# Optimization experiments

Measured on AMD Instinct MI355X. Metric: run time of the kernel, lower is better.

Reference implementation:

```python
import jax, jax.numpy as jnp
import numpy as np

EMBED_DIM = 384
MAX_LEN = 5000
TIMESTEP = 10000.0


def _build_table():
    pos = np.arange(MAX_LEN, dtype=np.float32)[:, None]
    div = np.exp(np.arange(0, EMBED_DIM, 2, dtype=np.float32) * (-np.log(TIMESTEP) / EMBED_DIM))
    pe = np.zeros((MAX_LEN, EMBED_DIM), dtype=np.float32)
    pe[:, 0::2] = np.sin(pos * div)
    pe[:, 1::2] = np.cos(pos * div)
    return jnp.asarray(pe)


def setup_inputs() -> dict:
    key = jax.random.key(0)
    x = jax.random.randint(key, (32, 512), 0, 16, dtype=jnp.int32)  # per-token durations
    pos_enc = _build_table()  # (MAX_LEN, EMBED_DIM) learned-free sinusoidal table
    return {"x": x, "pos_enc": pos_enc}


def reference(x, pos_enc):
    # x: (B, N) int durations; output: (B, T, D), T = max row-total frames
    cs = jnp.cumsum(x, axis=1)                 # (B, N) cumulative frame counts
    total = cs[:, -1]                          # (B,) frames per row
    T = int(np.asarray(jnp.max(cs)))           # concrete max total frames (data-dep, eval eagerly)
    starts = cs - x                            # (B, N) start frame of each token
    t = jnp.arange(T, dtype=cs.dtype)          # (T,) frame indices
    # token owning each frame: first index with cs > t
    tok = jax.vmap(lambda c: jnp.searchsorted(c, t, side='right'))(cs)  # (B, T)
    tok = jnp.minimum(tok, x.shape[1] - 1)     # clamp for padded frames
    pos = t[None, :] - jnp.take_along_axis(starts, tok, axis=1)         # (B, T) within-token position
    valid = t[None, :] < total[:, None]        # (B, T)
    pos = jnp.where(valid, pos, 0)
    emb = pos_enc[pos]                         # (B, T, D) gather
    return emb * valid[..., None].astype(emb.dtype)
```

## Files before the change

### kernel.cpp

```cpp
#include <hip/hip_runtime.h>
#include <hip/hip_bf16.h>


#define B 32
#define L 512
#define D 384
#define D4 (D / 4)

__global__ __launch_bounds__(64) void pe_cumsum_kernel(
    const int* __restrict__ x, int* __restrict__ cs) {
  const int b = blockIdx.x;
  const int lane = threadIdx.x;
  const int base = b * L + lane * 8;

  const int4* xr = reinterpret_cast<const int4*>(x + base);
  int4 a = xr[0];
  int4 c = xr[1];
  int v[8] = {a.x, a.y, a.z, a.w, c.x, c.y, c.z, c.w};

  int pref[8];
  int s = 0;
#pragma unroll
  for (int k = 0; k < 8; ++k) { s += v[k]; pref[k] = s; }

  int acc = s;
#pragma unroll
  for (int off = 1; off < 64; off <<= 1) {
    int n = __shfl_up(acc, off);
    if (lane >= off) acc += n;
  }
  const int offset = acc - s;

  int4 o0 = make_int4(offset + pref[0], offset + pref[1],
                      offset + pref[2], offset + pref[3]);
  int4 o1 = make_int4(offset + pref[4], offset + pref[5],
                      offset + pref[6], offset + pref[7]);
  int4* cr = reinterpret_cast<int4*>(cs + base);
  cr[0] = o0;
  cr[1] = o1;
}

__global__ __launch_bounds__(256) void pe_searchsorted_kernel(
    const int* __restrict__ x, const int* __restrict__ cs,
    int* __restrict__ posidx, int T) {
  const int b = blockIdx.y;
  const int t = blockIdx.x * 256 + threadIdx.x;
  if (t >= T) return;

  const int* csr = cs + b * L;
  const int total = csr[L - 1];

  int out = -1;
  if (t < total) {
    int lo = 0, hi = L;
    while (lo < hi) {
      int mid = (lo + hi) >> 1;
      if (csr[mid] <= t) lo = mid + 1; else hi = mid;
    }
    int tok = lo < (L - 1) ? lo : (L - 1);
    out = t - (csr[tok] - x[b * L + tok]);
  }
  posidx[b * T + t] = out;
}

__global__ __launch_bounds__(256) void pe_gather_kernel(
    const float4* __restrict__ pe, const int* __restrict__ posidx,
    float4* __restrict__ out, int n4) {
  const int stride = gridDim.x * blockDim.x;
  for (int i = blockIdx.x * blockDim.x + threadIdx.x; i < n4; i += stride) {
    const int row = i / D4;
    const int col = i - row * D4;
    const int p = posidx[row];
    float4 v = make_float4(0.f, 0.f, 0.f, 0.f);
    if (p >= 0) v = pe[p * D4 + col];
    out[i] = v;
  }
}

extern "C" void kernel_launch(void* const* d_in, const int* in_sizes, int n_in,
                              void* d_out, int out_size, void* d_ws, size_t ws_size,
                              hipStream_t stream) {
  const int* x = (const int*)d_in[0];
  const float* pe = (const float*)d_in[1];
  float* out = (float*)d_out;

  const int T = out_size / (B * D);

  int* cs = (int*)d_ws;
  int* posidx = cs + B * L;

  pe_cumsum_kernel<<<B, 64, 0, stream>>>(x, cs);

  dim3 g2((T + 255) / 256, B);
  pe_searchsorted_kernel<<<g2, 256, 0, stream>>>(x, cs, posidx, T);

  const int n4 = out_size / 4;
  int blocks = (n4 + 255) / 256;
  if (blocks > 2048) blocks = 2048;
  pe_gather_kernel<<<blocks, 256, 0, stream>>>(
      (const float4*)pe, posidx, (float4*)out, n4);
}
```

Before: 200.9 us.

## Replace searchsorted+gather with per-token segment copy and tail zeroing

Instead of computing a per-frame token index by binary search and then gathering table rows, each (batch, token) block copies the first c rows of the positional table directly into that token's output segment. A separate kernel zeros the padded frames past each row's total. This removes the index buffer, the binary searches and the per-element index loads. It trades them for many small blocks with uneven work and unaligned segment starts.

```diff
diff --git a/kernel.cpp b/kernel.cpp
--- a/kernel.cpp
+++ b/kernel.cpp
@@ -40,40 +40,32 @@
   cr[1] = o1;
 }
 
-__global__ __launch_bounds__(256) void pe_searchsorted_kernel(
+__global__ __launch_bounds__(256) void pe_segcopy_kernel(
     const int* __restrict__ x, const int* __restrict__ cs,
-    int* __restrict__ posidx, int T) {
+    const float4* __restrict__ pe, float4* __restrict__ out, int T) {
+  const int j = blockIdx.x;
   const int b = blockIdx.y;
-  const int t = blockIdx.x * 256 + threadIdx.x;
-  if (t >= T) return;
+  const int c = x[b * L + j];
+  if (c == 0) return;
+  const int start = cs[b * L + j] - c;
 
-  const int* csr = cs + b * L;
-  const int total = csr[L - 1];
-
-  int out = -1;
-  if (t < total) {
-    int lo = 0, hi = L;
-    while (lo < hi) {
-      int mid = (lo + hi) >> 1;
-      if (csr[mid] <= t) lo = mid + 1; else hi = mid;
-    }
-    int tok = lo < (L - 1) ? lo : (L - 1);
-    out = t - (csr[tok] - x[b * L + tok]);
+  float4* dst = out + ((size_t)b * T + start) * D4;
+  const int n = c * D4;
+  for (int i = threadIdx.x; i < n; i += 256) {
+    dst[i] = pe[i];
   }
-  posidx[b * T + t] = out;
 }
 
-__global__ __launch_bounds__(256) void pe_gather_kernel(
-    const float4* __restrict__ pe, const int* __restrict__ posidx,
-    float4* __restrict__ out, int n4) {
-  const int stride = gridDim.x * blockDim.x;
-  for (int i = blockIdx.x * blockDim.x + threadIdx.x; i < n4; i += stride) {
-    const int row = i / D4;
-    const int col = i - row * D4;
-    const int p = posidx[row];
-    float4 v = make_float4(0.f, 0.f, 0.f, 0.f);
-    if (p >= 0) v = pe[p * D4 + col];
-    out[i] = v;
+__global__ __launch_bounds__(256) void pe_tailzero_kernel(
+    const int* __restrict__ cs, float4* __restrict__ out, int T) {
+  const int b = blockIdx.y;
+  const int total = cs[b * L + (L - 1)];
+  const int n = (T - total) * D4;
+  float4* dst = out + ((size_t)b * T + total) * D4;
+  const float4 z = make_float4(0.f, 0.f, 0.f, 0.f);
+  const int stride = gridDim.x * 256;
+  for (int i = blockIdx.x * 256 + threadIdx.x; i < n; i += stride) {
+    dst[i] = z;
   }
 }
 
@@ -87,16 +79,13 @@
   const int T = out_size / (B * D);
 
   int* cs = (int*)d_ws;
-  int* posidx = cs + B * L;
 
   pe_cumsum_kernel<<<B, 64, 0, stream>>>(x, cs);
 
-  dim3 g2((T + 255) / 256, B);
-  pe_searchsorted_kernel<<<g2, 256, 0, stream>>>(x, cs, posidx, T);
+  dim3 g2(L, B);
+  pe_segcopy_kernel<<<g2, 256, 0, stream>>>(x, cs, (const float4*)pe,
+                                            (float4*)out, T);
 
-  const int n4 = out_size / 4;
-  int blocks = (n4 + 255) / 256;
-  if (blocks > 2048) blocks = 2048;
-  pe_gather_kernel<<<blocks, 256, 0, stream>>>(
-      (const float4*)pe, posidx, (float4*)out, n4);
+  dim3 g3(32, B);
+  pe_tailzero_kernel<<<g3, 256, 0, stream>>>(cs, (float4*)out, T);
 }
```

After: 202.1 us. Within noise of the previous version (+0.6%).
